# Kernel tuning notes

Hardware: AMD Instinct MI355X
Metric: run time of the kernel (lower is better)

The kernel has to match this reference:

```python
import jax, jax.numpy as jnp
import numpy as np

B, T, E = 4, 2048, 512
H, D = 8, 64            # num_heads, head_size = E // H
HID = H * E             # FFN hidden = num_heads * n_embed (per source)
EPS = 1e-5


def layer_norm(x, g, b):
    mu = jnp.mean(x, axis=-1, keepdims=True)
    var = jnp.var(x, axis=-1, keepdims=True)
    return (x - mu) * jax.lax.rsqrt(var + EPS) * g + b


def setup_inputs() -> dict:
    key = jax.random.key(0)
    ks = jax.random.split(key, 12)
    s_e = 1.0 / np.sqrt(E)
    s_hd = 1.0 / np.sqrt(H * D)
    s_hid = 1.0 / np.sqrt(HID)
    return {
        "x": jax.random.normal(ks[0], (B, T, E), jnp.float32),
        "Wq": jax.random.normal(ks[1], (H, E, D), jnp.float32) * s_e,
        "Wk": jax.random.normal(ks[2], (H, E, D), jnp.float32) * s_e,
        "Wv": jax.random.normal(ks[3], (H, E, D), jnp.float32) * s_e,
        "Wo": jax.random.normal(ks[4], (H * D, E), jnp.float32) * s_hd,
        "bo": jnp.zeros((E,), jnp.float32),
        "W1": jax.random.normal(ks[5], (E, HID), jnp.float32) * s_e,
        "b1": jnp.zeros((HID,), jnp.float32),
        "W2": jax.random.normal(ks[6], (HID, E), jnp.float32) * s_hid,
        "b2": jnp.zeros((E,), jnp.float32),
        "g1": jnp.ones((E,), jnp.float32),
        "be1": jnp.zeros((E,), jnp.float32),
        "g2": jnp.ones((E,), jnp.float32),
        "be2": jnp.zeros((E,), jnp.float32),
    }


def reference(x, Wq, Wk, Wv, Wo, bo, W1, b1, W2, b2, g1, be1, g2, be2):
    # pre-LN decoder block (layer_norm_first=True path)
    xn = layer_norm(x, g1, be1)

    # multi-head causal attention; NOTE: scale is T**-0.5 per the source code
    q = jnp.einsum('bte,hed->bhtd', xn, Wq)
    k = jnp.einsum('bte,hed->bhtd', xn, Wk)
    v = jnp.einsum('bte,hed->bhtd', xn, Wv)
    scores = jnp.einsum('bhtd,bhsd->bhts', q, k) * (T ** -0.5)
    causal = jnp.tril(jnp.ones((T, T), bool))
    scores = jnp.where(causal, scores, -jnp.inf)
    attn = jax.nn.softmax(scores, axis=-1)
    o = jnp.einsum('bhts,bhsd->bhtd', attn, v)           # [B,H,T,D]
    o = o.transpose(0, 2, 1, 3).reshape(B, T, H * D)      # concat heads
    mha = o @ Wo + bo

    x = xn + mha
    xn2 = layer_norm(x, g2, be2)
    ffn = jax.nn.relu(xn2 @ W1 + b1) @ W2 + b2
    return xn2 + ffn
```

## Files before the change

kernel.cpp:

```cpp
#include <hip/hip_runtime.h>
#include <hip/hip_bf16.h>
#include <math.h>

#define Bsz 4
#define Tt 2048
#define Ee 512
#define Hh 8
#define Dd 64
#define HIDs 4096
#define Mrows (Bsz * Tt)

typedef __attribute__((ext_vector_type(8))) short short8;
typedef __attribute__((ext_vector_type(4))) float f32x4;
typedef __attribute__((ext_vector_type(16))) float f32x16;

#define AS1 __attribute__((address_space(1)))
#define AS3 __attribute__((address_space(3)))

__device__ __forceinline__ unsigned short f2bfu(float f) {
    unsigned u = __float_as_uint(f);
    return (unsigned short)((u + 0x7fffu + ((u >> 16) & 1u)) >> 16);
}
__device__ __forceinline__ unsigned short truncbf(float f) {
    return (unsigned short)(__float_as_uint(f) >> 16);
}

__device__ __forceinline__ void ln_body(const float* __restrict__ x,
        const float* __restrict__ g, const float* __restrict__ b,
        const float* __restrict__ addb,
        float* __restrict__ out_f, __hip_bfloat16* __restrict__ out_bf,
        int row) {
    int tid = threadIdx.x;
    const float* xr = x + (size_t)row * Ee;
    float v0 = xr[tid];
    float v1 = xr[tid + 256];
    float s = v0 + v1;
    float sq = v0 * v0 + v1 * v1;
#pragma unroll
    for (int off = 32; off > 0; off >>= 1) {
        s  += __shfl_xor(s, off, 64);
        sq += __shfl_xor(sq, off, 64);
    }
    __shared__ float ls[4], lq[4];
    int wid = tid >> 6, lane = tid & 63;
    if (lane == 0) { ls[wid] = s; lq[wid] = sq; }
    __syncthreads();
    s  = ls[0] + ls[1] + ls[2] + ls[3];
    sq = lq[0] + lq[1] + lq[2] + lq[3];
    float mean = s * (1.0f / Ee);
    float var  = sq * (1.0f / Ee) - mean * mean;
    float rstd = rsqrtf(var + 1e-5f);
    float o0 = (v0 - mean) * rstd * g[tid]       + b[tid];
    float o1 = (v1 - mean) * rstd * g[tid + 256] + b[tid + 256];
    float* orow = out_f + (size_t)row * Ee;
    orow[tid]       = o0 + addb[tid];
    orow[tid + 256] = o1 + addb[tid + 256];
    __hip_bfloat16* brow = out_bf + (size_t)row * Ee;
    brow[tid]       = __float2bfloat16(o0);
    brow[tid + 256] = __float2bfloat16(o1);
}

__global__ __launch_bounds__(256) void ln_kernel(const float* __restrict__ x,
        const float* __restrict__ g, const float* __restrict__ b,
        const float* __restrict__ addb,
        float* __restrict__ out_f, __hip_bfloat16* __restrict__ out_bf) {
    ln_body(x, g, b, addb, out_f, out_bf, blockIdx.x);
}

__device__ __forceinline__ void tr_tile(const float* __restrict__ in,
        __hip_bfloat16* __restrict__ outp, int R, int C, int c0, int r0) {
    __shared__ float tile[64][65];
    int tc = threadIdx.x & 63, tg = threadIdx.x >> 6;
#pragma unroll
    for (int i = 0; i < 16; ++i) {
        int r = tg * 16 + i;
        tile[r][tc] = in[(size_t)(r0 + r) * C + c0 + tc];
    }
    __syncthreads();
#pragma unroll
    for (int i = 0; i < 16; ++i) {
        int cc = tg * 16 + i;
        outp[(size_t)(c0 + cc) * R + r0 + tc] = __float2bfloat16(tile[tc][cc]);
    }
}
__global__ __launch_bounds__(256) void startup_kernel(
        const float* __restrict__ x, const float* __restrict__ g1,
        const float* __restrict__ be1, const float* __restrict__ bo,
        float* __restrict__ xn, __hip_bfloat16* __restrict__ xn_bf,
        const float* __restrict__ Wq, const float* __restrict__ Wk,
        const float* __restrict__ Wv, const float* __restrict__ Wo,
        const float* __restrict__ W1, const float* __restrict__ W2,
        __hip_bfloat16* __restrict__ bqT, __hip_bfloat16* __restrict__ woT,
        __hip_bfloat16* __restrict__ w1T, __hip_bfloat16* __restrict__ w2T) {
    if (blockIdx.x < Mrows) {
        ln_body(x, g1, be1, bo, xn, xn_bf, blockIdx.x);
        return;
    }
    int blk = blockIdx.x - Mrows;
    if (blk < 192) {
        int p = blk >> 6, h = (blk >> 3) & 7, et = blk & 7;
        const float* W = (p == 0) ? Wq : ((p == 1) ? Wk : Wv);
        float sc = (p == 0) ? 0.022097086912079608f * 1.4426950408889634f : 1.0f;
        __shared__ float tile[64][65];
        int td = threadIdx.x & 63, tg = threadIdx.x >> 6;
#pragma unroll
        for (int i = 0; i < 16; ++i) {
            int e = tg * 16 + i;
            tile[e][td] = W[((size_t)h * Ee + et * 64 + e) * Dd + td] * sc;
        }
        __syncthreads();
#pragma unroll
        for (int i = 0; i < 16; ++i) {
            int d = tg * 16 + i;
            bqT[((size_t)(p * 512 + h * 64 + d)) * Ee + et * 64 + td] =
                __float2bfloat16(tile[td][d]);
        }
    } else if (blk < 256) {
        int t = blk - 192;
        tr_tile(Wo, woT, 512, 512, (t & 7) * 64, (t >> 3) * 64);
    } else if (blk < 768) {
        int t = blk - 256;
        tr_tile(W1, w1T, 512, HIDs, (t & 63) * 64, (t >> 6) * 64);
    } else {
        int t = blk - 768;
        tr_tile(W2, w2T, HIDs, 512, (t & 7) * 64, (t >> 3) * 64);
    }
}

__global__ __launch_bounds__(256) void mfma_gemm(
        const __hip_bfloat16* __restrict__ A, int lda,
        const __hip_bfloat16* __restrict__ B, int ldb,
        __hip_bfloat16* __restrict__ Cb, int ldc, int K, int nx) {
    __shared__ __hip_bfloat16 S[16384];
    __hip_bfloat16* As = S;
    __hip_bfloat16* Bs = S + 8192;
    int tid = threadIdx.x;
    int lane = tid & 63, wave = tid >> 6;
    int wm = wave >> 1, wn = wave & 1;
    int L = blockIdx.x;
    int slots = (int)gridDim.x >> 3;
    int v = (L & 7) * slots + (L >> 3);
    int bx = v % nx, by = v / nx;
    int row0 = by * 128, col0 = bx * 128;
    f32x4 acc[4][4];
#pragma unroll
    for (int i = 0; i < 4; ++i)
#pragma unroll
        for (int j = 0; j < 4; ++j) acc[i][j] = (f32x4){0.f, 0.f, 0.f, 0.f};

    int fr = lane & 15;
    int kq = (lane >> 4) << 3;

    for (int k0 = 0; k0 < K; k0 += 64) {
        __syncthreads();
#pragma unroll
        for (int j = 0; j < 4; ++j) {
            int c  = j * 256 + tid;
            int cb = j * 256 + wave * 64;
            int p  = c >> 9, cp = c & 511;
            int r  = cp >> 2, kg = (cp & 3) << 3;
            int ko = k0 + p * 32 + kg;
            __builtin_amdgcn_global_load_lds(
                (const AS1 void*)(A + (size_t)(row0 + r) * lda + ko),
                (AS3 void*)(As + cb * 8), 16, 0, 0);
            __builtin_amdgcn_global_load_lds(
                (const AS1 void*)(B + (size_t)(col0 + r) * ldb + ko),
                (AS3 void*)(Bs + cb * 8), 16, 0, 0);
        }
        __syncthreads();
#pragma unroll
        for (int ks = 0; ks < 2; ++ks) {
            short8 afr[4], bfr[4];
#pragma unroll
            for (int i = 0; i < 4; ++i) {
                afr[i] = *(const short8*)(As + ks * 4096 + (wm * 64 + i * 16 + fr) * 32 + kq);
                bfr[i] = *(const short8*)(Bs + ks * 4096 + (wn * 64 + i * 16 + fr) * 32 + kq);
            }
#pragma unroll
            for (int i = 0; i < 4; ++i)
#pragma unroll
                for (int j = 0; j < 4; ++j)
                    acc[i][j] = __builtin_amdgcn_mfma_f32_16x16x32_bf16(afr[i], bfr[j], acc[i][j], 0, 0, 0);
        }
    }
    __syncthreads();
    unsigned short* Ew = (unsigned short*)S + wave * 1152;
    const __hip_bfloat16* Er = (const __hip_bfloat16*)Ew;
    int rq = (lane >> 4) << 2;
    int rr = lane >> 2, cb2 = (lane & 3) * 16;
#pragma unroll
    for (int i = 0; i < 4; ++i) {
#pragma unroll
        for (int j = 0; j < 4; ++j)
#pragma unroll
            for (int gi = 0; gi < 4; ++gi)
                Ew[(rq + gi) * 72 + j * 16 + fr] = f2bfu(acc[i][j][gi]);
        uint4 v0 = *(const uint4*)(Er + rr * 72 + cb2);
        uint4 v1 = *(const uint4*)(Er + rr * 72 + cb2 + 8);
        size_t rg = (size_t)(row0 + wm * 64 + i * 16 + rr) * ldc + col0 + wn * 64 + cb2;
        *(uint4*)(Cb + rg)     = v0;
        *(uint4*)(Cb + rg + 8) = v1;
    }
}

__global__ __launch_bounds__(256) void mfma_gemm_n64(
        const __hip_bfloat16* __restrict__ A, int lda,
        const __hip_bfloat16* __restrict__ B, int ldb,
        float* __restrict__ Cf, int ldc, int K, int nx) {
    __shared__ __hip_bfloat16 As[2 * 128 * 32];
    __shared__ __hip_bfloat16 Bs[2 * 64 * 32];
    int tid = threadIdx.x;
    int lane = tid & 63, wave = tid >> 6;
    int L = blockIdx.x;
    int slots = (int)gridDim.x >> 3;
    int v = (L & 7) * slots + (L >> 3);
    int bx = v % nx, by = v / nx;
    int row0 = by * 128, col0 = bx * 64;
    f32x4 acc[2][4];
#pragma unroll
    for (int i = 0; i < 2; ++i)
#pragma unroll
        for (int j = 0; j < 4; ++j) acc[i][j] = (f32x4){0.f, 0.f, 0.f, 0.f};

    int fr = lane & 15;
    int kq = (lane >> 4) << 3;

    for (int k0 = 0; k0 < K; k0 += 64) {
        __syncthreads();
#pragma unroll
        for (int j = 0; j < 4; ++j) {
            int c  = j * 256 + tid;
            int cb = j * 256 + wave * 64;
            int p  = c >> 9, cp = c & 511;
            int r  = cp >> 2, kg = (cp & 3) << 3;
            __builtin_amdgcn_global_load_lds(
                (const AS1 void*)(A + (size_t)(row0 + r) * lda + k0 + p * 32 + kg),
                (AS3 void*)(As + cb * 8), 16, 0, 0);
        }
#pragma unroll
        for (int j = 0; j < 2; ++j) {
            int c  = j * 256 + tid;
            int cb = j * 256 + wave * 64;
            int p  = c >> 8, cp = c & 255;
            int r  = cp >> 2, kg = (cp & 3) << 3;
            __builtin_amdgcn_global_load_lds(
                (const AS1 void*)(B + (size_t)(col0 + r) * ldb + k0 + p * 32 + kg),
                (AS3 void*)(Bs + cb * 8), 16, 0, 0);
        }
        __syncthreads();
#pragma unroll
        for (int ks = 0; ks < 2; ++ks) {
            short8 afr[2], bfr[4];
#pragma unroll
            for (int i = 0; i < 2; ++i)
                afr[i] = *(const short8*)(As + ks * 4096 + (wave * 32 + i * 16 + fr) * 32 + kq);
#pragma unroll
            for (int j = 0; j < 4; ++j)
                bfr[j] = *(const short8*)(Bs + ks * 2048 + (j * 16 + fr) * 32 + kq);
#pragma unroll
            for (int i = 0; i < 2; ++i)
#pragma unroll
                for (int j = 0; j < 4; ++j)
                    acc[i][j] = __builtin_amdgcn_mfma_f32_16x16x32_bf16(afr[i], bfr[j], acc[i][j], 0, 0, 0);
        }
    }
    int rq = (lane >> 4) << 2;
#pragma unroll
    for (int i = 0; i < 2; ++i)
#pragma unroll
        for (int j = 0; j < 4; ++j)
#pragma unroll
            for (int gidx = 0; gidx < 4; ++gidx) {
                int r = row0 + wave * 32 + i * 16 + rq + gidx;
                int c = col0 + j * 16 + fr;
                Cf[(size_t)r * ldc + c] += acc[i][j][gidx];
            }
}

__device__ __forceinline__ short8 ld_frag(const __hip_bfloat16* base, int r, int slot) {
    return *(const short8*)(base + r * 64 + ((slot ^ (r & 7)) << 3));
}

__global__ __launch_bounds__(512, 2) void gemm256_8ph(
        const __hip_bfloat16* __restrict__ A, int lda,
        const __hip_bfloat16* __restrict__ B, int ldb,
        __hip_bfloat16* __restrict__ Cb, int ldc, int K,
        const float* __restrict__ bias, int nx) {
    __shared__ __hip_bfloat16 S[65536];
    __hip_bfloat16* Asb = S;
    __hip_bfloat16* Bsb = S + 32768;
    int tid = threadIdx.x;
    int lane = tid & 63, wave = tid >> 6;
    int wm = wave >> 2, wn = wave & 3;
    int fr = lane & 15, l5 = lane >> 4;
    int L = blockIdx.x;
    int slots = (int)gridDim.x >> 3;
    int v = (L & 7) * slots + (L >> 3);
    int bx = v % nx, by = v / nx;
    int row0 = by * 256, col0 = bx * 256;
    int T = K >> 6;

    f32x4 acc[8][4];
#pragma unroll
    for (int i = 0; i < 8; ++i)
#pragma unroll
        for (int j = 0; j < 4; ++j) acc[i][j] = (f32x4){0.f, 0.f, 0.f, 0.f};

#define STAGE_A(tt, hh, bb)                                                   \
    do {                                                                      \
        _Pragma("unroll")                                                     \
        for (int j = 0; j < 2; ++j) {                                         \
            int c = j * 512 + tid;                                            \
            int r = c >> 3;                                                   \
            int sl = (c & 7) ^ (r & 7);                                       \
            int cb = j * 512 + wave * 64;                                     \
            int grow = row0 + ((r >> 6) << 7) + (hh) * 64 + (r & 63);         \
            __builtin_amdgcn_global_load_lds(                                 \
                (const AS1 void*)(A + (size_t)grow * lda + (tt) * 64 + sl * 8), \
                (AS3 void*)(Asb + (bb) * 16384 + (hh) * 8192 + cb * 8), 16, 0, 0); \
        }                                                                     \
    } while (0)
#define STAGE_B(tt, hh, bb)                                                   \
    do {                                                                      \
        _Pragma("unroll")                                                     \
        for (int j = 0; j < 2; ++j) {                                         \
            int c = j * 512 + tid;                                            \
            int r = c >> 3;                                                   \
            int sl = (c & 7) ^ (r & 7);                                       \
            int cb = j * 512 + wave * 64;                                     \
            int gcol = col0 + ((r >> 5) << 6) + (hh) * 32 + (r & 31);         \
            __builtin_amdgcn_global_load_lds(                                 \
                (const AS1 void*)(B + (size_t)gcol * ldb + (tt) * 64 + sl * 8), \
                (AS3 void*)(Bsb + (bb) * 16384 + (hh) * 8192 + cb * 8), 16, 0, 0); \
        }                                                                     \
    } while (0)

    STAGE_A(0, 0, 0);
    STAGE_B(0, 0, 0);
    STAGE_B(0, 1, 0);
    STAGE_A(0, 1, 0);

    short8 a[4][2], b[2][2][2];
    for (int t = 0; t < T; ++t) {
        int buf = t & 1, nb = buf ^ 1;
        int tn = (t + 1 < T) ? t + 1 : 0;
        const __hip_bfloat16* Ab0 = Asb + buf * 16384;
        const __hip_bfloat16* Ab1 = Ab0 + 8192;
        const __hip_bfloat16* Bb0 = Bsb + buf * 16384;
        const __hip_bfloat16* Bb1 = Bb0 + 8192;

        STAGE_A(tn, 0, nb);
        asm volatile("s_waitcnt vmcnt(6)" ::: "memory");
        __builtin_amdgcn_s_barrier();
        asm volatile("" ::: "memory");
#pragma unroll
        for (int i = 0; i < 4; ++i)
#pragma unroll
            for (int ks = 0; ks < 2; ++ks)
                a[i][ks] = ld_frag(Ab0, wm * 64 + i * 16 + fr, ks * 4 + l5);
#pragma unroll
        for (int jj = 0; jj < 2; ++jj)
#pragma unroll
            for (int ks = 0; ks < 2; ++ks)
                b[0][jj][ks] = ld_frag(Bb0, wn * 32 + jj * 16 + fr, ks * 4 + l5);
        __builtin_amdgcn_s_setprio(1);
#pragma unroll
        for (int i = 0; i < 4; ++i)
#pragma unroll
            for (int jj = 0; jj < 2; ++jj)
#pragma unroll
                for (int ks = 0; ks < 2; ++ks)
                    acc[i][jj] = __builtin_amdgcn_mfma_f32_16x16x32_bf16(
                        a[i][ks], b[0][jj][ks], acc[i][jj], 0, 0, 0);
        __builtin_amdgcn_s_setprio(0);
        asm volatile("" ::: "memory");
        __builtin_amdgcn_s_barrier();
        asm volatile("" ::: "memory");

        STAGE_B(tn, 0, nb);
        asm volatile("s_waitcnt vmcnt(6)" ::: "memory");
        __builtin_amdgcn_s_barrier();
        asm volatile("" ::: "memory");
#pragma unroll
        for (int jj = 0; jj < 2; ++jj)
#pragma unroll
            for (int ks = 0; ks < 2; ++ks)
                b[1][jj][ks] = ld_frag(Bb1, wn * 32 + jj * 16 + fr, ks * 4 + l5);
        __builtin_amdgcn_s_setprio(1);
#pragma unroll
        for (int i = 0; i < 4; ++i)
#pragma unroll
            for (int jj = 0; jj < 2; ++jj)
#pragma unroll
                for (int ks = 0; ks < 2; ++ks)
                    acc[i][2 + jj] = __builtin_amdgcn_mfma_f32_16x16x32_bf16(
                        a[i][ks], b[1][jj][ks], acc[i][2 + jj], 0, 0, 0);
        __builtin_amdgcn_s_setprio(0);
        asm volatile("" ::: "memory");
        __builtin_amdgcn_s_barrier();
        asm volatile("" ::: "memory");

        STAGE_B(tn, 1, nb);
        asm volatile("s_waitcnt vmcnt(6)" ::: "memory");
        __builtin_amdgcn_s_barrier();
        asm volatile("" ::: "memory");
#pragma unroll
        for (int i = 0; i < 4; ++i)
#pragma unroll
            for (int ks = 0; ks < 2; ++ks)
                a[i][ks] = ld_frag(Ab1, wm * 64 + i * 16 + fr, ks * 4 + l5);
        __builtin_amdgcn_s_setprio(1);
#pragma unroll
        for (int i = 0; i < 4; ++i)
#pragma unroll
            for (int jj = 0; jj < 2; ++jj)
#pragma unroll
                for (int ks = 0; ks < 2; ++ks)
                    acc[4 + i][2 + jj] = __builtin_amdgcn_mfma_f32_16x16x32_bf16(
                        a[i][ks], b[1][jj][ks], acc[4 + i][2 + jj], 0, 0, 0);
        __builtin_amdgcn_s_setprio(0);
        asm volatile("" ::: "memory");
        __builtin_amdgcn_s_barrier();
        asm volatile("" ::: "memory");

        STAGE_A(tn, 1, nb);
        asm volatile("" ::: "memory");
        __builtin_amdgcn_s_barrier();
        asm volatile("" ::: "memory");
        __builtin_amdgcn_s_setprio(1);
#pragma unroll
        for (int i = 0; i < 4; ++i)
#pragma unroll
            for (int jj = 0; jj < 2; ++jj)
#pragma unroll
                for (int ks = 0; ks < 2; ++ks)
                    acc[4 + i][jj] = __builtin_amdgcn_mfma_f32_16x16x32_bf16(
                        a[i][ks], b[0][jj][ks], acc[4 + i][jj], 0, 0, 0);
        __builtin_amdgcn_s_setprio(0);
        asm volatile("" ::: "memory");
        __builtin_amdgcn_s_barrier();
        asm volatile("" ::: "memory");
    }
#undef STAGE_A
#undef STAGE_B

    __syncthreads();
    float bvv[4];
#pragma unroll
    for (int nj = 0; nj < 4; ++nj) bvv[nj] = bias[col0 + wn * 64 + nj * 16 + fr];
    unsigned short* Ew = (unsigned short*)S + wave * 1152;
    const __hip_bfloat16* Er = (const __hip_bfloat16*)Ew;
    int rq = l5 << 2;
    int rr = lane >> 2, cb2 = (lane & 3) * 16;
#pragma unroll
    for (int mi = 0; mi < 8; ++mi) {
#pragma unroll
        for (int nj = 0; nj < 4; ++nj)
#pragma unroll
            for (int gi = 0; gi < 4; ++gi) {
                float tv = acc[mi][nj][gi] + bvv[nj];
                Ew[(rq + gi) * 72 + nj * 16 + fr] = f2bfu(tv > 0.f ? tv : 0.f);
            }
        uint4 v0 = *(const uint4*)(Er + rr * 72 + cb2);
        uint4 v1 = *(const uint4*)(Er + rr * 72 + cb2 + 8);
        size_t rg = (size_t)(row0 + wm * 128 + mi * 16 + rr) * ldc
                    + col0 + wn * 64 + cb2;
        *(uint4*)(Cb + rg)     = v0;
        *(uint4*)(Cb + rg + 8) = v1;
    }
}

__global__ __launch_bounds__(256) void attn_mfma(const __hip_bfloat16* __restrict__ qkvb,
        __hip_bfloat16* __restrict__ ob) {
    __shared__ __hip_bfloat16 KsS[2][64 * 72];
    __shared__ __hip_bfloat16 VtS[2][64 * 72];
    __shared__ __hip_bfloat16 PsS[4 * 32 * 72];
    __hip_bfloat16* Qs = PsS;

    const unsigned short* q16 = (const unsigned short*)qkvb;
    int tid  = threadIdx.x;
    int lane = tid & 63, wave = tid >> 6;
    int l31 = lane & 31, l5 = lane >> 5;
    int blk = blockIdx.x;
    int qb  = 15 - (blk >> 5);
    int bh  = blk & 31;
    int b = bh >> 3, h = bh & 7;
    int base = qb * 128;
    size_t tokbase = (size_t)b * Tt;
    int qoff = h * 64, koff = 512 + h * 64, voff = 1024 + h * 64;

    {
        int q = tid >> 1, dg = (tid & 1) * 32;
        const unsigned short* src = q16 + (tokbase + base + q) * 1536 + qoff + dg;
        uint4 a  = *(const uint4*)src;
        uint4 b4 = *(const uint4*)(src + 8);
        uint4 c4 = *(const uint4*)(src + 16);
        uint4 d4 = *(const uint4*)(src + 24);
        *(uint4*)(Qs + q * 72 + dg)      = a;
        *(uint4*)(Qs + q * 72 + dg + 8)  = b4;
        *(uint4*)(Qs + q * 72 + dg + 16) = c4;
        *(uint4*)(Qs + q * 72 + dg + 24) = d4;
    }
    __syncthreads();
    short8 aq[4];
#pragma unroll
    for (int kd = 0; kd < 4; ++kd)
        aq[kd] = *(const short8*)(Qs + (wave * 32 + l31) * 72 + kd * 16 + l5 * 8);

    short8 ones;
#pragma unroll
    for (int i = 0; i < 8; ++i) ones[i] = (short)0x3F80;

    f32x16 acc[2], accL;
#pragma unroll
    for (int i = 0; i < 16; ++i) { acc[0][i] = 0.f; acc[1][i] = 0.f; accL[i] = 0.f; }
    __hip_bfloat16* Psw = PsS + wave * (32 * 72);
    unsigned short* Psw16 = (unsigned short*)Psw;

    int s_k = tid >> 2, dg_k = (tid & 3) * 16;
    int sp = (tid & 31) * 2, dg8 = (tid >> 5) * 8;
    uint4 kr0, kr1, va, vb;
    {
        const unsigned short* kp = q16 + (tokbase + s_k) * 1536 + koff + dg_k;
        kr0 = *(const uint4*)kp;
        kr1 = *(const uint4*)(kp + 8);
        const unsigned short* vp = q16 + (tokbase + sp) * 1536 + voff + dg8;
        va = *(const uint4*)vp;
        vb = *(const uint4*)(vp + 1536);
    }

    int tmax = 2 * qb + 1;
    for (int tile = 0; tile <= tmax; ++tile) {
        int buf = tile & 1;
        *(uint4*)(KsS[buf] + s_k * 72 + dg_k)     = kr0;
        *(uint4*)(KsS[buf] + s_k * 72 + dg_k + 8) = kr1;
        {
            unsigned a0[4] = {va.x, va.y, va.z, va.w};
            unsigned b0[4] = {vb.x, vb.y, vb.z, vb.w};
#pragma unroll
            for (int i = 0; i < 4; ++i) {
                unsigned p0 = (a0[i] & 0xffffu) | (b0[i] << 16);
                unsigned p1 = (a0[i] >> 16) | (b0[i] & 0xffff0000u);
                *(unsigned*)(VtS[buf] + (dg8 + 2 * i) * 72 + sp)     = p0;
                *(unsigned*)(VtS[buf] + (dg8 + 2 * i + 1) * 72 + sp) = p1;
            }
        }
        __syncthreads();
        if (tile < tmax) {
            int s1 = (tile + 1) * 64;
            const unsigned short* kp = q16 + (tokbase + s1 + s_k) * 1536 + koff + dg_k;
            kr0 = *(const uint4*)kp;
            kr1 = *(const uint4*)(kp + 8);
            const unsigned short* vp = q16 + (tokbase + s1 + sp) * 1536 + voff + dg8;
            va = *(const uint4*)vp;
            vb = *(const uint4*)(vp + 1536);
        }
        if (tile == tmax && wave < 2) continue;
        f32x16 Sc[2];
#pragma unroll
        for (int i = 0; i < 16; ++i) { Sc[0][i] = 0.f; Sc[1][i] = 0.f; }
#pragma unroll
        for (int st = 0; st < 2; ++st)
#pragma unroll
            for (int kd = 0; kd < 4; ++kd) {
                short8 bk = *(const short8*)(KsS[buf] + (st * 32 + l31) * 72 + kd * 16 + l5 * 8);
                Sc[st] = __builtin_amdgcn_mfma_f32_32x32x16_bf16(aq[kd], bk, Sc[st], 0, 0, 0);
            }
        if (tile >= 2 * qb) {
            int s0t = tile * 64;
            int qrb = base + wave * 32 + 4 * l5;
#pragma unroll
            for (int st = 0; st < 2; ++st) {
                int sg = s0t + st * 32 + l31;
#pragma unroll
                for (int reg = 0; reg < 16; ++reg) {
                    int qr = qrb + (reg & 3) + 8 * (reg >> 2);
                    if (sg > qr) Sc[st][reg] = -1e30f;
                }
            }
        }
#pragma unroll
        for (int st = 0; st < 2; ++st)
#pragma unroll
            for (int reg = 0; reg < 16; ++reg) {
                int pr = (reg & 3) + 8 * (reg >> 2) + 4 * l5;
                Psw16[pr * 72 + st * 32 + l31] =
                    truncbf(__builtin_amdgcn_exp2f(Sc[st][reg]));
            }
#pragma unroll
        for (int ks = 0; ks < 4; ++ks) {
            short8 ap = *(const short8*)(Psw + l31 * 72 + ks * 16 + l5 * 8);
            accL = __builtin_amdgcn_mfma_f32_32x32x16_bf16(ap, ones, accL, 0, 0, 0);
#pragma unroll
            for (int dt = 0; dt < 2; ++dt) {
                short8 bv = *(const short8*)(VtS[buf] + (dt * 32 + l31) * 72 + ks * 16 + l5 * 8);
                acc[dt] = __builtin_amdgcn_mfma_f32_32x32x16_bf16(ap, bv, acc[dt], 0, 0, 0);
            }
        }
    }
#pragma unroll
    for (int reg = 0; reg < 16; ++reg) {
        float rl = 1.0f / accL[reg];
        int qr = base + wave * 32 + (reg & 3) + 8 * (reg >> 2) + 4 * l5;
#pragma unroll
        for (int dt = 0; dt < 2; ++dt)
            ob[(tokbase + qr) * 512 + h * 64 + dt * 32 + l31] =
                __float2bfloat16(acc[dt][reg] * rl);
    }
}

extern "C" void kernel_launch(void* const* d_in, const int* in_sizes, int n_in,
                              void* d_out, int out_size, void* d_ws, size_t ws_size,
                              hipStream_t stream) {
    const float* x   = (const float*)d_in[0];
    const float* Wq  = (const float*)d_in[1];
    const float* Wk  = (const float*)d_in[2];
    const float* Wv  = (const float*)d_in[3];
    const float* Wo  = (const float*)d_in[4];
    const float* bo  = (const float*)d_in[5];
    const float* W1  = (const float*)d_in[6];
    const float* b1  = (const float*)d_in[7];
    const float* W2  = (const float*)d_in[8];
    const float* b2  = (const float*)d_in[9];
    const float* g1  = (const float*)d_in[10];
    const float* be1 = (const float*)d_in[11];
    const float* g2  = (const float*)d_in[12];
    const float* be2 = (const float*)d_in[13];
    float* out = (float*)d_out;

    char* ws = (char*)d_ws;
    __hip_bfloat16* bqT    = (__hip_bfloat16*)(ws);
    __hip_bfloat16* woT    = (__hip_bfloat16*)(ws + 1572864);
    __hip_bfloat16* w1T    = (__hip_bfloat16*)(ws + 2097152);
    __hip_bfloat16* w2T    = (__hip_bfloat16*)(ws + 6291456);
    float*          xn     = (float*)(ws + 10485760);
    __hip_bfloat16* xn_bf  = (__hip_bfloat16*)(ws + 27262976);
    __hip_bfloat16* qkv_bf = (__hip_bfloat16*)(ws + 35651584);
    __hip_bfloat16* o_bf   = (__hip_bfloat16*)(ws + 60817408);
    __hip_bfloat16* h_bf   = (__hip_bfloat16*)(ws + 35651584);

    startup_kernel<<<Mrows + 1280, 256, 0, stream>>>(
        x, g1, be1, bo, xn, xn_bf, Wq, Wk, Wv, Wo, W1, W2, bqT, woT, w1T, w2T);
    mfma_gemm<<<768, 256, 0, stream>>>(
        xn_bf, 512, bqT, 512, qkv_bf, 1536, 512, 12);
    attn_mfma<<<Bsz * Hh * (Tt / 128), 256, 0, stream>>>(qkv_bf, o_bf);
    mfma_gemm_n64<<<512, 256, 0, stream>>>(
        o_bf, 512, woT, 512, xn, 512, 512, 8);
    ln_kernel<<<Mrows, 256, 0, stream>>>(xn, g2, be2, b2, out, xn_bf);
    gemm256_8ph<<<512, 512, 0, stream>>>(
        xn_bf, 512, w1T, 512, h_bf, HIDs, 512, b1, 16);
    mfma_gemm_n64<<<512, 256, 0, stream>>>(
        h_bf, HIDs, w2T, HIDs, out, 512, HIDs, 8);
}
```

Before: 308.4 us.

## Multi-buffer LDS staging with XOR swizzle in mfma_gemm and mfma_gemm_n64

The two smaller MFMA GEMM kernels now prefetch the next K tiles into LDS while computing on the current one. mfma_gemm uses two buffers and mfma_gemm_n64 uses three, with explicit vmcnt waits and raw barriers in place of __syncthreads. The LDS layout is also XOR-swizzled on the k-slot to reduce bank conflicts on fragment reads. The cost is more LDS per block, which can lower occupancy, and redundant dummy loads on the last iterations.

```diff
diff --git a/kernel.cpp b/kernel.cpp
--- a/kernel.cpp
+++ b/kernel.cpp
@@ -23,6 +23,10 @@
 }
 __device__ __forceinline__ unsigned short truncbf(float f) {
     return (unsigned short)(__float_as_uint(f) >> 16);
+}
+
+__device__ __forceinline__ short8 ld_sw(const __hip_bfloat16* base, int R, int sl) {
+    return *(const short8*)(base + R * 32 + (((sl) ^ ((R >> 1) & 3)) << 3));
 }
 
 __device__ __forceinline__ void ln_body(const float* __restrict__ x,
@@ -131,9 +135,7 @@
         const __hip_bfloat16* __restrict__ A, int lda,
         const __hip_bfloat16* __restrict__ B, int ldb,
         __hip_bfloat16* __restrict__ Cb, int ldc, int K, int nx) {
-    __shared__ __hip_bfloat16 S[16384];
-    __hip_bfloat16* As = S;
-    __hip_bfloat16* Bs = S + 8192;
+    __shared__ __hip_bfloat16 S[32768];
     int tid = threadIdx.x;
     int lane = tid & 63, wave = tid >> 6;
     int wm = wave >> 1, wn = wave & 1;
@@ -148,33 +150,45 @@
 #pragma unroll
         for (int j = 0; j < 4; ++j) acc[i][j] = (f32x4){0.f, 0.f, 0.f, 0.f};
 
-    int fr = lane & 15;
-    int kq = (lane >> 4) << 3;
-
-    for (int k0 = 0; k0 < K; k0 += 64) {
-        __syncthreads();
-#pragma unroll
-        for (int j = 0; j < 4; ++j) {
-            int c  = j * 256 + tid;
-            int cb = j * 256 + wave * 64;
-            int p  = c >> 9, cp = c & 511;
-            int r  = cp >> 2, kg = (cp & 3) << 3;
-            int ko = k0 + p * 32 + kg;
-            __builtin_amdgcn_global_load_lds(
-                (const AS1 void*)(A + (size_t)(row0 + r) * lda + ko),
-                (AS3 void*)(As + cb * 8), 16, 0, 0);
-            __builtin_amdgcn_global_load_lds(
-                (const AS1 void*)(B + (size_t)(col0 + r) * ldb + ko),
-                (AS3 void*)(Bs + cb * 8), 16, 0, 0);
-        }
-        __syncthreads();
+    int fr = lane & 15, sl = lane >> 4;
+    int T = K >> 6;
+
+#define STAGEQ(tt, bb)                                                        \
+    do {                                                                      \
+        int kk_ = (tt) * 64;                                                  \
+        _Pragma("unroll")                                                     \
+        for (int j = 0; j < 4; ++j) {                                         \
+            int c = j * 256 + tid;                                            \
+            int p = c >> 9, cp = c & 511;                                     \
+            int r = cp >> 2, s = cp & 3;                                      \
+            int kg = ((s ^ ((r >> 1) & 3)) << 3);                             \
+            int cb = j * 256 + wave * 64;                                     \
+            int ko = kk_ + p * 32 + kg;                                       \
+            __builtin_amdgcn_global_load_lds(                                 \
+                (const AS1 void*)(A + (size_t)(row0 + r) * lda + ko),         \
+                (AS3 void*)(S + (bb) * 16384 + cb * 8), 16, 0, 0);            \
+            __builtin_amdgcn_global_load_lds(                                 \
+                (const AS1 void*)(B + (size_t)(col0 + r) * ldb + ko),         \
+                (AS3 void*)(S + (bb) * 16384 + 8192 + cb * 8), 16, 0, 0);     \
+        }                                                                     \
+    } while (0)
+
+    STAGEQ(0, 0);
+    for (int t = 0; t < T; ++t) {
+        int tn = (t + 1 < T) ? t + 1 : 0;
+        STAGEQ(tn, (t + 1) & 1);
+        asm volatile("s_waitcnt vmcnt(8)" ::: "memory");
+        __builtin_amdgcn_s_barrier();
+        asm volatile("" ::: "memory");
+        const __hip_bfloat16* Ab = S + (t & 1) * 16384;
+        const __hip_bfloat16* Bb = Ab + 8192;
 #pragma unroll
         for (int ks = 0; ks < 2; ++ks) {
             short8 afr[4], bfr[4];
 #pragma unroll
             for (int i = 0; i < 4; ++i) {
-                afr[i] = *(const short8*)(As + ks * 4096 + (wm * 64 + i * 16 + fr) * 32 + kq);
-                bfr[i] = *(const short8*)(Bs + ks * 4096 + (wn * 64 + i * 16 + fr) * 32 + kq);
+                afr[i] = ld_sw(Ab + ks * 4096, wm * 64 + i * 16 + fr, sl);
+                bfr[i] = ld_sw(Bb + ks * 4096, wn * 64 + i * 16 + fr, sl);
             }
 #pragma unroll
             for (int i = 0; i < 4; ++i)
@@ -182,7 +196,12 @@
                 for (int j = 0; j < 4; ++j)
                     acc[i][j] = __builtin_amdgcn_mfma_f32_16x16x32_bf16(afr[i], bfr[j], acc[i][j], 0, 0, 0);
         }
-    }
+        asm volatile("" ::: "memory");
+        __builtin_amdgcn_s_barrier();
+        asm volatile("" ::: "memory");
+    }
+#undef STAGEQ
+    asm volatile("s_waitcnt vmcnt(0)" ::: "memory");
     __syncthreads();
     unsigned short* Ew = (unsigned short*)S + wave * 1152;
     const __hip_bfloat16* Er = (const __hip_bfloat16*)Ew;
@@ -207,8 +226,7 @@
         const __hip_bfloat16* __restrict__ A, int lda,
         const __hip_bfloat16* __restrict__ B, int ldb,
         float* __restrict__ Cf, int ldc, int K, int nx) {
-    __shared__ __hip_bfloat16 As[2 * 128 * 32];
-    __shared__ __hip_bfloat16 Bs[2 * 64 * 32];
+    __shared__ __hip_bfloat16 S[36864];
     int tid = threadIdx.x;
     int lane = tid & 63, wave = tid >> 6;
     int L = blockIdx.x;
@@ -222,48 +240,67 @@
 #pragma unroll
         for (int j = 0; j < 4; ++j) acc[i][j] = (f32x4){0.f, 0.f, 0.f, 0.f};
 
-    int fr = lane & 15;
-    int kq = (lane >> 4) << 3;
-
-    for (int k0 = 0; k0 < K; k0 += 64) {
-        __syncthreads();
-#pragma unroll
-        for (int j = 0; j < 4; ++j) {
-            int c  = j * 256 + tid;
-            int cb = j * 256 + wave * 64;
-            int p  = c >> 9, cp = c & 511;
-            int r  = cp >> 2, kg = (cp & 3) << 3;
-            __builtin_amdgcn_global_load_lds(
-                (const AS1 void*)(A + (size_t)(row0 + r) * lda + k0 + p * 32 + kg),
-                (AS3 void*)(As + cb * 8), 16, 0, 0);
-        }
-#pragma unroll
-        for (int j = 0; j < 2; ++j) {
-            int c  = j * 256 + tid;
-            int cb = j * 256 + wave * 64;
-            int p  = c >> 8, cp = c & 255;
-            int r  = cp >> 2, kg = (cp & 3) << 3;
-            __builtin_amdgcn_global_load_lds(
-                (const AS1 void*)(B + (size_t)(col0 + r) * ldb + k0 + p * 32 + kg),
-                (AS3 void*)(Bs + cb * 8), 16, 0, 0);
-        }
-        __syncthreads();
+    int fr = lane & 15, sl = lane >> 4;
+    int T = K >> 6;
+
+#define STAGEN(tt, bb)                                                        \
+    do {                                                                      \
+        int kk_ = (tt) * 64;                                                  \
+        _Pragma("unroll")                                                     \
+        for (int j = 0; j < 4; ++j) {                                         \
+            int c = j * 256 + tid;                                            \
+            int p = c >> 9, cp = c & 511;                                     \
+            int r = cp >> 2, s = cp & 3;                                      \
+            int kg = ((s ^ ((r >> 1) & 3)) << 3);                             \
+            int cb = j * 256 + wave * 64;                                     \
+            __builtin_amdgcn_global_load_lds(                                 \
+                (const AS1 void*)(A + (size_t)(row0 + r) * lda + kk_ + p * 32 + kg), \
+                (AS3 void*)(S + (bb) * 12288 + cb * 8), 16, 0, 0);            \
+        }                                                                     \
+        _Pragma("unroll")                                                     \
+        for (int j = 0; j < 2; ++j) {                                         \
+            int c = j * 256 + tid;                                            \
+            int p = c >> 8, cp = c & 255;                                     \
+            int r = cp >> 2, s = cp & 3;                                      \
+            int kg = ((s ^ ((r >> 1) & 3)) << 3);                             \
+            int cb = j * 256 + wave * 64;                                     \
+            __builtin_amdgcn_global_load_lds(                                 \
+                (const AS1 void*)(B + (size_t)(col0 + r) * ldb + kk_ + p * 32 + kg), \
+                (AS3 void*)(S + (bb) * 12288 + 8192 + cb * 8), 16, 0, 0);     \
+        }                                                                     \
+    } while (0)
+
+    STAGEN(0, 0);
+    STAGEN(1, 1);
+    for (int t = 0; t < T; ++t) {
+        int tn = (t + 2 < T) ? t + 2 : 0;
+        STAGEN(tn, (t + 2) % 3);
+        asm volatile("s_waitcnt vmcnt(12)" ::: "memory");
+        __builtin_amdgcn_s_barrier();
+        asm volatile("" ::: "memory");
+        const __hip_bfloat16* Ab = S + (t % 3) * 12288;
+        const __hip_bfloat16* Bb = Ab + 8192;
 #pragma unroll
         for (int ks = 0; ks < 2; ++ks) {
             short8 afr[2], bfr[4];
 #pragma unroll
             for (int i = 0; i < 2; ++i)
-                afr[i] = *(const short8*)(As + ks * 4096 + (wave * 32 + i * 16 + fr) * 32 + kq);
+                afr[i] = ld_sw(Ab + ks * 4096, wave * 32 + i * 16 + fr, sl);
 #pragma unroll
             for (int j = 0; j < 4; ++j)
-                bfr[j] = *(const short8*)(Bs + ks * 2048 + (j * 16 + fr) * 32 + kq);
+                bfr[j] = ld_sw(Bb + ks * 2048, j * 16 + fr, sl);
 #pragma unroll
             for (int i = 0; i < 2; ++i)
 #pragma unroll
                 for (int j = 0; j < 4; ++j)
                     acc[i][j] = __builtin_amdgcn_mfma_f32_16x16x32_bf16(afr[i], bfr[j], acc[i][j], 0, 0, 0);
         }
-    }
+        asm volatile("" ::: "memory");
+        __builtin_amdgcn_s_barrier();
+        asm volatile("" ::: "memory");
+    }
+#undef STAGEN
+    asm volatile("s_waitcnt vmcnt(0)" ::: "memory");
     int rq = (lane >> 4) << 2;
 #pragma unroll
     for (int i = 0; i < 2; ++i)
```

Result: faster. 301.1 us (median of 5 runs) (-2.4%).
